# Performance work log

Hardware: AMD Instinct MI355X
Metric: run time of the kernel (lower is better)

Reference implementation:

```python
import jax, jax.numpy as jnp
import numpy as np

DIM = 1024
N_HEADS = 16
HEAD_DIM = DIM // N_HEADS


def setup_inputs() -> dict:
    key = jax.random.key(0)
    ks = jax.random.split(key, 5)
    s = 1.0 / np.sqrt(DIM)
    return {
        "x": jax.random.normal(ks[0], (2, 2048, DIM), dtype=jnp.float32),
        "w_qkv": jax.random.normal(ks[1], (DIM, 3 * DIM), dtype=jnp.float32) * s,
        "b_qkv": jnp.zeros((3 * DIM,), dtype=jnp.float32),
        "w_proj": jax.random.normal(ks[2], (DIM, DIM), dtype=jnp.float32) * s,
        "b_proj": jnp.zeros((DIM,), dtype=jnp.float32),
    }


def reference(x, w_qkv, b_qkv, w_proj, b_proj):
    B, T, C = x.shape
    qkv = x @ w_qkv + b_qkv                      # [B,T,3C]
    qkv = qkv.reshape(B, T, 3, N_HEADS, HEAD_DIM)
    q, k, v = qkv[:, :, 0], qkv[:, :, 1], qkv[:, :, 2]  # [B,T,H,D]
    scale = 1.0 / np.sqrt(HEAD_DIM)
    scores = jnp.einsum("bqhd,bkhd->bhqk", q, k) * scale  # [B,H,T,T]
    attn = jax.nn.softmax(scores, axis=-1)
    out = jnp.einsum("bhqk,bkhd->bqhd", attn, v)          # [B,T,H,D]
    out = out.reshape(B, T, C)
    return out @ w_proj + b_proj
```

## Files before the change

### kernel.cpp

```cpp
#include <hip/hip_runtime.h>

typedef unsigned short u16;
typedef unsigned int   u32;
typedef __bf16 bf16x8 __attribute__((ext_vector_type(8)));
typedef float  f32x4  __attribute__((ext_vector_type(4)));
typedef float  f32x16 __attribute__((ext_vector_type(16)));

#define TSEQ 2048
#define NHEAD 16
#define HDIM 64
#define CDIM 1024
#define N3   3072
#define MROWS 4096

__device__ __forceinline__ u16 f2bf(float f) {
    union { float f; u32 u; } v; v.f = f;
    u32 r = v.u + 0x7FFFu + ((v.u >> 16) & 1u);
    return (u16)(r >> 16);
}

__device__ __forceinline__ u32 pkbf(float a, float b) {
#if __has_builtin(__builtin_amdgcn_cvt_pk_bf16_f32)
    typedef __bf16 bf16x2 __attribute__((ext_vector_type(2)));
    bf16x2 t = __builtin_amdgcn_cvt_pk_bf16_f32(a, b);
    union { bf16x2 v; u32 u; } c; c.v = t; return c.u;
#else
    union { float f; u32 u; } ua, ub; ua.f = a; ub.f = b;
    u32 sel = 0x07060302, d;
    asm("v_perm_b32 %0, %1, %2, %3" : "=v"(d) : "v"(ub.u), "v"(ua.u), "v"(sel));
    return d;
#endif
}

__device__ __forceinline__ void gld16(const u16* g, u16* l) {
    __builtin_amdgcn_global_load_lds(
        (const __attribute__((address_space(1))) u32*)g,
        (__attribute__((address_space(3))) u32*)l, 16, 0, 0);
}

__global__ __launch_bounds__(256) void pack_bf16_kernel(const float* __restrict__ in,
                                                        u16* __restrict__ out, int n4) {
    int i = blockIdx.x * 256 + threadIdx.x;
    if (i >= n4) return;
    float4 v = reinterpret_cast<const float4*>(in)[i];
    ushort4 o;
    o.x = f2bf(v.x); o.y = f2bf(v.y); o.z = f2bf(v.z); o.w = f2bf(v.w);
    reinterpret_cast<ushort4*>(out)[i] = o;
}

__global__ __launch_bounds__(256) void transpose_pack2(const float* __restrict__ wqkv,
                                                       const float* __restrict__ wproj,
                                                       u16* __restrict__ oqkv, u16* __restrict__ oproj) {
    __shared__ float tile[32][33];
    const int bx = blockIdx.x;
    const float* in; u16* out; int N, n0;
    if (bx < 96) { in = wqkv;  out = oqkv;  N = 3072; n0 = bx * 32; }
    else         { in = wproj; out = oproj; N = 1024; n0 = (bx - 96) * 32; }
    int k0 = blockIdx.y * 32;
    int tx = threadIdx.x, ty = threadIdx.y;
#pragma unroll
    for (int i = 0; i < 4; i++)
        tile[ty + i * 8][tx] = in[(size_t)(k0 + ty + i * 8) * N + n0 + tx];
    __syncthreads();
#pragma unroll
    for (int i = 0; i < 4; i++)
        out[(size_t)(n0 + ty + i * 8) * 1024 + k0 + tx] = f2bf(tile[tx][ty + i * 8]);
}

__global__ __launch_bounds__(256) void gemm_qkv(const u16* __restrict__ A, const u16* __restrict__ Bt,
                                                const float* __restrict__ bias, u16* __restrict__ Qf,
                                                u16* __restrict__ Kf, u16* __restrict__ Vf) {
    __shared__ __align__(16) u16 Al[128 * 32];
    __shared__ __align__(16) u16 Bl[128 * 32];
    __shared__ __align__(16) u16 Im[16384];
    const int tid  = threadIdx.x;
    const int lane = tid & 63;
    const int wave = tid >> 6;
    const int wm = (wave >> 1) * 64;
    const int wn = (wave & 1) * 64;
    const int row0 = blockIdx.x * 128;
    const int col0 = blockIdx.y * 128;
    const int lr = lane & 15;
    const int lq = lane >> 4;
    const float c2 = 0.125f * 1.44269504088896f;

    f32x4 acc[4][4];
#pragma unroll
    for (int i = 0; i < 4; i++)
#pragma unroll
        for (int j = 0; j < 4; j++) acc[i][j] = f32x4{0.f, 0.f, 0.f, 0.f};

    const int sr = tid >> 2, sc_ = (tid & 3) * 8;

    for (int k0 = 0; k0 < CDIM; k0 += 32) {
#pragma unroll
        for (int s = 0; s < 2; s++) {
            int i = tid + s * 256;
            int r = sr + s * 64;
            gld16(&A[(size_t)(row0 + r) * CDIM + k0 + sc_], &Al[i * 8]);
            gld16(&Bt[(size_t)(col0 + r) * CDIM + k0 + sc_], &Bl[i * 8]);
        }
        __syncthreads();
        bf16x8 af[4], bfr[4];
#pragma unroll
        for (int t = 0; t < 4; t++) {
            af[t]  = *reinterpret_cast<const bf16x8*>(&Al[(wm + t * 16 + lr) * 32 + lq * 8]);
            bfr[t] = *reinterpret_cast<const bf16x8*>(&Bl[(wn + t * 16 + lr) * 32 + lq * 8]);
        }
#pragma unroll
        for (int mt = 0; mt < 4; mt++)
#pragma unroll
            for (int nt = 0; nt < 4; nt++)
                acc[mt][nt] = __builtin_amdgcn_mfma_f32_16x16x32_bf16(af[mt], bfr[nt], acc[mt][nt], 0, 0, 0);
        __syncthreads();
    }

    const int region = col0 >> 10;
    const int h_base = (col0 & 1023) >> 6;
#pragma unroll
    for (int mt = 0; mt < 4; mt++) {
#pragma unroll
        for (int nt = 0; nt < 4; nt++) {
            int n_local = wn + nt * 16 + lr;
            float bv = bias[col0 + n_local];
            int h_local = n_local >> 6;
            int d = n_local & 63;
#pragma unroll
            for (int r = 0; r < 4; r++) {
                int m_local = wm + mt * 16 + lq * 4 + r;
                float v = acc[mt][nt][r] + bv;
                if (region == 0) {
                    int qt_local = m_local >> 5, q31 = m_local & 31;
                    int kc = d >> 4, l5b = (d >> 3) & 1, j = d & 7;
                    int lc = (h_local * 4 + qt_local) * 4 + kc;
                    Im[lc * 512 + (l5b * 32 + q31) * 8 + j] = f2bf(v * c2);
                } else if (region == 1) {
                    int kb_local = m_local >> 6, tr = m_local & 63;
                    int kc = d >> 4, l5b = (d >> 3) & 1, j = d & 7;
                    int nt2 = tr >> 5, p31 = tr & 31;
                    int lc = (h_local * 2 + kb_local) * 8 + kc * 2 + nt2;
                    Im[lc * 512 + (l5b * 32 + p31) * 8 + j] = f2bf(v);
                } else {
                    int kb_local = m_local >> 6, tr = m_local & 63;
                    int cV = tr >> 4, dt2 = d >> 5, p31 = d & 31;
                    int l5b = (tr >> 2) & 1;
                    int j = ((tr >> 3) & 1) * 4 + (tr & 3);
                    int lc = (h_local * 2 + kb_local) * 8 + cV * 2 + dt2;
                    Im[lc * 512 + (l5b * 32 + p31) * 8 + j] = f2bf(v);
                }
            }
        }
    }
    __syncthreads();
    const int bq = row0 >> 11;
    const int qrow0 = row0 & 2047;
#pragma unroll
    for (int s = 0; s < 8; s++) {
        int slot = s * 256 + tid;
        int lc = slot >> 6, li = slot & 63;
        uint4 data = *reinterpret_cast<const uint4*>(&Im[slot * 8]);
        if (region == 0) {
            int h_local = lc >> 4, qt_local = (lc >> 2) & 3, kc = lc & 3;
            size_t off = ((size_t)((bq * 16 + h_base + h_local) * 64 + (qrow0 >> 5) + qt_local) * 4 + kc) * 512
                       + li * 8;
            *reinterpret_cast<uint4*>(Qf + off) = data;
        } else {
            int h_local = lc >> 4, kb_local = (lc >> 3) & 1, cit = lc & 7;
            size_t off = (size_t)((bq * 16 + h_base + h_local) * 32 + (qrow0 >> 6) + kb_local) * 4096
                       + cit * 512 + li * 8;
            *reinterpret_cast<uint4*>((region == 1 ? Kf : Vf) + off) = data;
        }
    }
}

__global__ __launch_bounds__(256) void gemm_proj(const u16* __restrict__ A, const u16* __restrict__ Bt,
                                                 const float* __restrict__ bias, float* __restrict__ C) {
    __shared__ __align__(16) u16 Al[64 * 32];
    __shared__ __align__(16) u16 Bl[128 * 32];
    const int tid  = threadIdx.x;
    const int lane = tid & 63;
    const int wave = tid >> 6;
    const int wm = (wave >> 1) * 32;
    const int wn = (wave & 1) * 64;
    const int row0 = blockIdx.x * 64;
    const int col0 = blockIdx.y * 128;
    const int lr = lane & 15;
    const int lq = lane >> 4;

    f32x4 acc[2][4];
#pragma unroll
    for (int i = 0; i < 2; i++)
#pragma unroll
        for (int j = 0; j < 4; j++) acc[i][j] = f32x4{0.f, 0.f, 0.f, 0.f};

    const int sr = tid >> 2, sc_ = (tid & 3) * 8;

    for (int k0 = 0; k0 < CDIM; k0 += 32) {
        gld16(&A[(size_t)(row0 + sr) * CDIM + k0 + sc_], &Al[tid * 8]);
#pragma unroll
        for (int s = 0; s < 2; s++)
            gld16(&Bt[(size_t)(col0 + sr + s * 64) * CDIM + k0 + sc_], &Bl[(tid + s * 256) * 8]);
        __syncthreads();
        bf16x8 af[2], bfr[4];
#pragma unroll
        for (int t = 0; t < 2; t++)
            af[t] = *reinterpret_cast<const bf16x8*>(&Al[(wm + t * 16 + lr) * 32 + lq * 8]);
#pragma unroll
        for (int t = 0; t < 4; t++)
            bfr[t] = *reinterpret_cast<const bf16x8*>(&Bl[(wn + t * 16 + lr) * 32 + lq * 8]);
#pragma unroll
        for (int mt = 0; mt < 2; mt++)
#pragma unroll
            for (int nt = 0; nt < 4; nt++)
                acc[mt][nt] = __builtin_amdgcn_mfma_f32_16x16x32_bf16(af[mt], bfr[nt], acc[mt][nt], 0, 0, 0);
        __syncthreads();
    }
#pragma unroll
    for (int mt = 0; mt < 2; mt++) {
#pragma unroll
        for (int nt = 0; nt < 4; nt++) {
            int col = col0 + wn + nt * 16 + lr;
            float bv = bias[col];
#pragma unroll
            for (int r = 0; r < 4; r++) {
                int row = row0 + wm + mt * 16 + lq * 4 + r;
                C[(size_t)row * CDIM + col] = acc[mt][nt][r] + bv;
            }
        }
    }
}

__global__ __launch_bounds__(256) void attn_kernel(const u16* __restrict__ Qf,
                                                   const u16* __restrict__ Kf,
                                                   const u16* __restrict__ Vf,
                                                   u16* __restrict__ AO) {
    const int id = blockIdx.x;
    const int bh = id & 31;
    const int qb = id >> 5;
    const int b = bh >> 4, h = bh & 15;
    const int tid = threadIdx.x, lane = tid & 63, wave = tid >> 6;
    const int l31 = lane & 31, l5 = lane >> 5;
    const int qt = qb * 4 + wave;
    const int q0 = qt * 32;

    bf16x8 qf[4];
    {
        const u16* qp = Qf + ((size_t)(bh * 64 + qt) * 4) * 512 + lane * 8;
#pragma unroll
        for (int kc = 0; kc < 4; kc++) qf[kc] = *reinterpret_cast<const bf16x8*>(qp + kc * 512);
    }
    f32x16 o[2];
    f32x16 zc;
#pragma unroll
    for (int i = 0; i < 16; i++) { o[0][i] = 0.f; o[1][i] = 0.f; zc[i] = 0.f; }
    float l = 0.f;

    const u16* kcur = Kf + (size_t)bh * 32 * 4096 + lane * 8;
    const u16* vcur = Vf + (size_t)bh * 32 * 4096 + lane * 8;

    bf16x8 ka[8];
#pragma unroll
    for (int i = 0; i < 8; i++) ka[i] = *reinterpret_cast<const bf16x8*>(kcur + i * 512);

    for (int kb = 0; kb < 32; kb++) {
        f32x16 st[2];
        st[0] = __builtin_amdgcn_mfma_f32_32x32x16_bf16(ka[0], qf[0], zc, 0, 0, 0);
        st[1] = __builtin_amdgcn_mfma_f32_32x32x16_bf16(ka[1], qf[0], zc, 0, 0, 0);
#pragma unroll
        for (int kc = 1; kc < 4; kc++) {
            st[0] = __builtin_amdgcn_mfma_f32_32x32x16_bf16(ka[kc * 2],     qf[kc], st[0], 0, 0, 0);
            st[1] = __builtin_amdgcn_mfma_f32_32x32x16_bf16(ka[kc * 2 + 1], qf[kc], st[1], 0, 0, 0);
        }
        bf16x8 vfr[8];
#pragma unroll
        for (int i = 0; i < 8; i++) vfr[i] = *reinterpret_cast<const bf16x8*>(vcur + i * 512);
        const u16* knext = kcur + (kb < 31 ? 4096 : 0);
#pragma unroll
        for (int i = 0; i < 8; i++) ka[i] = *reinterpret_cast<const bf16x8*>(knext + i * 512);
        kcur = knext;
        vcur += 4096;
        bf16x8 pa[4];
#pragma unroll
        for (int nt = 0; nt < 2; nt++) {
            float pe[16];
#pragma unroll
            for (int r = 0; r < 16; r++) {
                pe[r] = __builtin_amdgcn_exp2f(st[nt][r]);
                l += pe[r];
            }
            union { bf16x8 v; u32 w[4]; } u0, u1;
#pragma unroll
            for (int j = 0; j < 4; j++) {
                u0.w[j] = pkbf(pe[2 * j],     pe[2 * j + 1]);
                u1.w[j] = pkbf(pe[8 + 2 * j], pe[8 + 2 * j + 1]);
            }
            pa[nt * 2]     = u0.v;
            pa[nt * 2 + 1] = u1.v;
        }
#pragma unroll
        for (int c = 0; c < 4; c++) {
            o[0] = __builtin_amdgcn_mfma_f32_32x32x16_bf16(pa[c], vfr[c * 2],     o[0], 0, 0, 0);
            o[1] = __builtin_amdgcn_mfma_f32_32x32x16_bf16(pa[c], vfr[c * 2 + 1], o[1], 0, 0, 0);
        }
    }
    l += __shfl_xor(l, 32);
    float linv = 1.0f / l;
#pragma unroll
    for (int reg = 0; reg < 16; reg++) {
        int qrow = (reg & 3) + 8 * (reg >> 2) + 4 * l5;
        float li = __shfl(linv, qrow);
#pragma unroll
        for (int dt = 0; dt < 2; dt++) {
            AO[(size_t)(b * TSEQ + q0 + qrow) * CDIM + h * 64 + dt * 32 + l31] =
                f2bf(o[dt][reg] * li);
        }
    }
}

extern "C" void kernel_launch(void* const* d_in, const int* in_sizes, int n_in,
                              void* d_out, int out_size, void* d_ws, size_t ws_size,
                              hipStream_t stream) {
    const float* x      = (const float*)d_in[0];
    const float* w_qkv  = (const float*)d_in[1];
    const float* b_qkv  = (const float*)d_in[2];
    const float* w_proj = (const float*)d_in[3];
    const float* b_proj = (const float*)d_in[4];
    float* out = (float*)d_out;

    u16* ws     = (u16*)d_ws;
    u16* Xb     = ws;
    u16* Wqkvt  = Xb + 4194304;
    u16* Wprojt = Wqkvt + 3145728;
    u16* Qf     = Wprojt + 1048576;
    u16* Kf     = Qf + 4194304;
    u16* Vf     = Kf + 4194304;
    u16* AO     = Vf + 4194304;

    pack_bf16_kernel<<<4096, 256, 0, stream>>>(x, Xb, 4194304 / 4);
    transpose_pack2<<<dim3(128, 32), dim3(32, 8), 0, stream>>>(w_qkv, w_proj, Wqkvt, Wprojt);
    gemm_qkv<<<dim3(32, 24), 256, 0, stream>>>(Xb, Wqkvt, b_qkv, Qf, Kf, Vf);
    attn_kernel<<<512, 256, 0, stream>>>(Qf, Kf, Vf, AO);
    gemm_proj<<<dim3(64, 8), 256, 0, stream>>>(AO, Wprojt, b_proj, out);
}
```

Before: 184.1 us.

## Process two query tiles per attention wave and merge prep kernels

Each attention wave now handles two 32-row query tiles and shares every K/V register fragment load between them. This halves the global K/V traffic per output and halves the grid to 256 blocks with launch_bounds occupancy hint 1. The input cast and the weight transpose/pack kernels are merged into one launch to save a launch. The cost is higher register pressure and fewer blocks than the 256 CUs can fully overlap, which may leave less latency hiding.

```diff
diff --git a/kernel.cpp b/kernel.cpp
--- a/kernel.cpp
+++ b/kernel.cpp
@@ -38,26 +38,29 @@
         (__attribute__((address_space(3))) u32*)l, 16, 0, 0);
 }
 
-__global__ __launch_bounds__(256) void pack_bf16_kernel(const float* __restrict__ in,
-                                                        u16* __restrict__ out, int n4) {
-    int i = blockIdx.x * 256 + threadIdx.x;
-    if (i >= n4) return;
-    float4 v = reinterpret_cast<const float4*>(in)[i];
-    ushort4 o;
-    o.x = f2bf(v.x); o.y = f2bf(v.y); o.z = f2bf(v.z); o.w = f2bf(v.w);
-    reinterpret_cast<ushort4*>(out)[i] = o;
-}
-
-__global__ __launch_bounds__(256) void transpose_pack2(const float* __restrict__ wqkv,
-                                                       const float* __restrict__ wproj,
-                                                       u16* __restrict__ oqkv, u16* __restrict__ oproj) {
+__global__ __launch_bounds__(256) void prep_kernel(const float* __restrict__ x,
+                                                   const float* __restrict__ wqkv,
+                                                   const float* __restrict__ wproj,
+                                                   u16* __restrict__ Xb,
+                                                   u16* __restrict__ oqkv, u16* __restrict__ oproj) {
     __shared__ float tile[32][33];
     const int bx = blockIdx.x;
+    const int tid = threadIdx.x;
+    if (bx < 4096) {
+        int i = bx * 256 + tid;
+        float4 v = reinterpret_cast<const float4*>(x)[i];
+        ushort4 o;
+        o.x = f2bf(v.x); o.y = f2bf(v.y); o.z = f2bf(v.z); o.w = f2bf(v.w);
+        reinterpret_cast<ushort4*>(Xb)[i] = o;
+        return;
+    }
+    int idx = bx - 4096;
+    int bnx = idx & 127;
+    int k0  = (idx >> 7) * 32;
     const float* in; u16* out; int N, n0;
-    if (bx < 96) { in = wqkv;  out = oqkv;  N = 3072; n0 = bx * 32; }
-    else         { in = wproj; out = oproj; N = 1024; n0 = (bx - 96) * 32; }
-    int k0 = blockIdx.y * 32;
-    int tx = threadIdx.x, ty = threadIdx.y;
+    if (bnx < 96) { in = wqkv;  out = oqkv;  N = 3072; n0 = bnx * 32; }
+    else          { in = wproj; out = oproj; N = 1024; n0 = (bnx - 96) * 32; }
+    int tx = tid & 31, ty = tid >> 5;
 #pragma unroll
     for (int i = 0; i < 4; i++)
         tile[ty + i * 8][tx] = in[(size_t)(k0 + ty + i * 8) * N + n0 + tx];
@@ -230,30 +233,31 @@
     }
 }
 
-__global__ __launch_bounds__(256) void attn_kernel(const u16* __restrict__ Qf,
-                                                   const u16* __restrict__ Kf,
-                                                   const u16* __restrict__ Vf,
-                                                   u16* __restrict__ AO) {
+__global__ __launch_bounds__(256, 1) void attn_kernel(const u16* __restrict__ Qf,
+                                                      const u16* __restrict__ Kf,
+                                                      const u16* __restrict__ Vf,
+                                                      u16* __restrict__ AO) {
     const int id = blockIdx.x;
     const int bh = id & 31;
     const int qb = id >> 5;
     const int b = bh >> 4, h = bh & 15;
     const int tid = threadIdx.x, lane = tid & 63, wave = tid >> 6;
     const int l31 = lane & 31, l5 = lane >> 5;
-    const int qt = qb * 4 + wave;
-    const int q0 = qt * 32;
-
-    bf16x8 qf[4];
+    const int qt0 = qb * 8 + wave * 2;
+
+    bf16x8 qa0[4], qa1[4];
     {
-        const u16* qp = Qf + ((size_t)(bh * 64 + qt) * 4) * 512 + lane * 8;
-#pragma unroll
-        for (int kc = 0; kc < 4; kc++) qf[kc] = *reinterpret_cast<const bf16x8*>(qp + kc * 512);
-    }
-    f32x16 o[2];
-    f32x16 zc;
-#pragma unroll
-    for (int i = 0; i < 16; i++) { o[0][i] = 0.f; o[1][i] = 0.f; zc[i] = 0.f; }
-    float l = 0.f;
+        const u16* qp = Qf + ((size_t)(bh * 64 + qt0) * 4) * 512 + lane * 8;
+#pragma unroll
+        for (int kc = 0; kc < 4; kc++) {
+            qa0[kc] = *reinterpret_cast<const bf16x8*>(qp + kc * 512);
+            qa1[kc] = *reinterpret_cast<const bf16x8*>(qp + 2048 + kc * 512);
+        }
+    }
+    f32x16 o00, o01, o10, o11, zc;
+#pragma unroll
+    for (int i = 0; i < 16; i++) { o00[i] = 0.f; o01[i] = 0.f; o10[i] = 0.f; o11[i] = 0.f; zc[i] = 0.f; }
+    float l0 = 0.f, l1 = 0.f;
 
     const u16* kcur = Kf + (size_t)bh * 32 * 4096 + lane * 8;
     const u16* vcur = Vf + (size_t)bh * 32 * 4096 + lane * 8;
@@ -263,13 +267,17 @@
     for (int i = 0; i < 8; i++) ka[i] = *reinterpret_cast<const bf16x8*>(kcur + i * 512);
 
     for (int kb = 0; kb < 32; kb++) {
-        f32x16 st[2];
-        st[0] = __builtin_amdgcn_mfma_f32_32x32x16_bf16(ka[0], qf[0], zc, 0, 0, 0);
-        st[1] = __builtin_amdgcn_mfma_f32_32x32x16_bf16(ka[1], qf[0], zc, 0, 0, 0);
+        f32x16 st00, st01, st10, st11;
+        st00 = __builtin_amdgcn_mfma_f32_32x32x16_bf16(ka[0], qa0[0], zc, 0, 0, 0);
+        st01 = __builtin_amdgcn_mfma_f32_32x32x16_bf16(ka[1], qa0[0], zc, 0, 0, 0);
+        st10 = __builtin_amdgcn_mfma_f32_32x32x16_bf16(ka[0], qa1[0], zc, 0, 0, 0);
+        st11 = __builtin_amdgcn_mfma_f32_32x32x16_bf16(ka[1], qa1[0], zc, 0, 0, 0);
 #pragma unroll
         for (int kc = 1; kc < 4; kc++) {
-            st[0] = __builtin_amdgcn_mfma_f32_32x32x16_bf16(ka[kc * 2],     qf[kc], st[0], 0, 0, 0);
-            st[1] = __builtin_amdgcn_mfma_f32_32x32x16_bf16(ka[kc * 2 + 1], qf[kc], st[1], 0, 0, 0);
+            st00 = __builtin_amdgcn_mfma_f32_32x32x16_bf16(ka[kc * 2],     qa0[kc], st00, 0, 0, 0);
+            st01 = __builtin_amdgcn_mfma_f32_32x32x16_bf16(ka[kc * 2 + 1], qa0[kc], st01, 0, 0, 0);
+            st10 = __builtin_amdgcn_mfma_f32_32x32x16_bf16(ka[kc * 2],     qa1[kc], st10, 0, 0, 0);
+            st11 = __builtin_amdgcn_mfma_f32_32x32x16_bf16(ka[kc * 2 + 1], qa1[kc], st11, 0, 0, 0);
         }
         bf16x8 vfr[8];
 #pragma unroll
@@ -279,40 +287,63 @@
         for (int i = 0; i < 8; i++) ka[i] = *reinterpret_cast<const bf16x8*>(knext + i * 512);
         kcur = knext;
         vcur += 4096;
-        bf16x8 pa[4];
-#pragma unroll
-        for (int nt = 0; nt < 2; nt++) {
+        bf16x8 pa0[4], pa1[4];
+        {
             float pe[16];
 #pragma unroll
-            for (int r = 0; r < 16; r++) {
-                pe[r] = __builtin_amdgcn_exp2f(st[nt][r]);
-                l += pe[r];
-            }
-            union { bf16x8 v; u32 w[4]; } u0, u1;
-#pragma unroll
-            for (int j = 0; j < 4; j++) {
-                u0.w[j] = pkbf(pe[2 * j],     pe[2 * j + 1]);
-                u1.w[j] = pkbf(pe[8 + 2 * j], pe[8 + 2 * j + 1]);
-            }
-            pa[nt * 2]     = u0.v;
-            pa[nt * 2 + 1] = u1.v;
+            for (int r = 0; r < 16; r++) { pe[r] = __builtin_amdgcn_exp2f(st00[r]); l0 += pe[r]; }
+            union { bf16x8 v; u32 w[4]; } ua, ub;
+#pragma unroll
+            for (int j = 0; j < 4; j++) { ua.w[j] = pkbf(pe[2 * j], pe[2 * j + 1]); ub.w[j] = pkbf(pe[8 + 2 * j], pe[8 + 2 * j + 1]); }
+            pa0[0] = ua.v; pa0[1] = ub.v;
+#pragma unroll
+            for (int r = 0; r < 16; r++) { pe[r] = __builtin_amdgcn_exp2f(st01[r]); l0 += pe[r]; }
+#pragma unroll
+            for (int j = 0; j < 4; j++) { ua.w[j] = pkbf(pe[2 * j], pe[2 * j + 1]); ub.w[j] = pkbf(pe[8 + 2 * j], pe[8 + 2 * j + 1]); }
+            pa0[2] = ua.v; pa0[3] = ub.v;
+#pragma unroll
+            for (int r = 0; r < 16; r++) { pe[r] = __builtin_amdgcn_exp2f(st10[r]); l1 += pe[r]; }
+#pragma unroll
+            for (int j = 0; j < 4; j++) { ua.w[j] = pkbf(pe[2 * j], pe[2 * j + 1]); ub.w[j] = pkbf(pe[8 + 2 * j], pe[8 + 2 * j + 1]); }
+            pa1[0] = ua.v; pa1[1] = ub.v;
+#pragma unroll
+            for (int r = 0; r < 16; r++) { pe[r] = __builtin_amdgcn_exp2f(st11[r]); l1 += pe[r]; }
+#pragma unroll
+            for (int j = 0; j < 4; j++) { ua.w[j] = pkbf(pe[2 * j], pe[2 * j + 1]); ub.w[j] = pkbf(pe[8 + 2 * j], pe[8 + 2 * j + 1]); }
+            pa1[2] = ua.v; pa1[3] = ub.v;
         }
 #pragma unroll
         for (int c = 0; c < 4; c++) {
-            o[0] = __builtin_amdgcn_mfma_f32_32x32x16_bf16(pa[c], vfr[c * 2],     o[0], 0, 0, 0);
-            o[1] = __builtin_amdgcn_mfma_f32_32x32x16_bf16(pa[c], vfr[c * 2 + 1], o[1], 0, 0, 0);
-        }
-    }
-    l += __shfl_xor(l, 32);
-    float linv = 1.0f / l;
-#pragma unroll
-    for (int reg = 0; reg < 16; reg++) {
-        int qrow = (reg & 3) + 8 * (reg >> 2) + 4 * l5;
-        float li = __shfl(linv, qrow);
-#pragma unroll
-        for (int dt = 0; dt < 2; dt++) {
-            AO[(size_t)(b * TSEQ + q0 + qrow) * CDIM + h * 64 + dt * 32 + l31] =
-                f2bf(o[dt][reg] * li);
+            o00 = __builtin_amdgcn_mfma_f32_32x32x16_bf16(pa0[c], vfr[c * 2],     o00, 0, 0, 0);
+            o01 = __builtin_amdgcn_mfma_f32_32x32x16_bf16(pa0[c], vfr[c * 2 + 1], o01, 0, 0, 0);
+            o10 = __builtin_amdgcn_mfma_f32_32x32x16_bf16(pa1[c], vfr[c * 2],     o10, 0, 0, 0);
+            o11 = __builtin_amdgcn_mfma_f32_32x32x16_bf16(pa1[c], vfr[c * 2 + 1], o11, 0, 0, 0);
+        }
+    }
+    {
+        float l = l0;
+        l += __shfl_xor(l, 32);
+        float linv = 1.0f / l;
+        int q0 = qt0 * 32;
+#pragma unroll
+        for (int reg = 0; reg < 16; reg++) {
+            int qrow = (reg & 3) + 8 * (reg >> 2) + 4 * l5;
+            float li = __shfl(linv, qrow);
+            AO[(size_t)(b * TSEQ + q0 + qrow) * CDIM + h * 64 + l31]      = f2bf(o00[reg] * li);
+            AO[(size_t)(b * TSEQ + q0 + qrow) * CDIM + h * 64 + 32 + l31] = f2bf(o01[reg] * li);
+        }
+    }
+    {
+        float l = l1;
+        l += __shfl_xor(l, 32);
+        float linv = 1.0f / l;
+        int q0 = (qt0 + 1) * 32;
+#pragma unroll
+        for (int reg = 0; reg < 16; reg++) {
+            int qrow = (reg & 3) + 8 * (reg >> 2) + 4 * l5;
+            float li = __shfl(linv, qrow);
+            AO[(size_t)(b * TSEQ + q0 + qrow) * CDIM + h * 64 + l31]      = f2bf(o10[reg] * li);
+            AO[(size_t)(b * TSEQ + q0 + qrow) * CDIM + h * 64 + 32 + l31] = f2bf(o11[reg] * li);
         }
     }
 }
@@ -336,9 +367,8 @@
     u16* Vf     = Kf + 4194304;
     u16* AO     = Vf + 4194304;
 
-    pack_bf16_kernel<<<4096, 256, 0, stream>>>(x, Xb, 4194304 / 4);
-    transpose_pack2<<<dim3(128, 32), dim3(32, 8), 0, stream>>>(w_qkv, w_proj, Wqkvt, Wprojt);
+    prep_kernel<<<8192, 256, 0, stream>>>(x, w_qkv, w_proj, Xb, Wqkvt, Wprojt);
     gemm_qkv<<<dim3(32, 24), 256, 0, stream>>>(Xb, Wqkvt, b_qkv, Qf, Kf, Vf);
-    attn_kernel<<<512, 256, 0, stream>>>(Qf, Kf, Vf, AO);
+    attn_kernel<<<256, 256, 0, stream>>>(Qf, Kf, Vf, AO);
     gemm_proj<<<dim3(64, 8), 256, 0, stream>>>(AO, Wprojt, b_proj, out);
 }
```

Result: faster. 175.5 us (-4.7%).
